# Performance work log

Measured on AMD Instinct MI355X. Metric: run time of the kernel, lower is better.

## Reference

```python
import jax, jax.numpy as jnp
import numpy as np
import math

B, T, D, H, TED = 32, 512, 512, 8, 2048
HD = D // H  # 64


def _ln(x, g, b, eps=1e-5):
    m = jnp.mean(x, axis=-1, keepdims=True)
    v = jnp.mean((x - m) ** 2, axis=-1, keepdims=True)
    return (x - m) * jax.lax.rsqrt(v + eps) * g + b


def setup_inputs() -> dict:
    key = jax.random.key(0)
    ks = jax.random.split(key, 12)
    s = 0.02
    return {
        "x": jax.random.normal(ks[0], (B, T, D), jnp.float32),
        "emb": jax.random.normal(ks[1], (B, TED), jnp.float32),
        "Wq": jax.random.normal(ks[2], (D, D), jnp.float32) * s,
        "Wk": jax.random.normal(ks[3], (D, D), jnp.float32) * s,
        "Wv": jax.random.normal(ks[4], (D, D), jnp.float32) * s,
        "Wsig": jax.random.normal(ks[5], (D, H), jnp.float32) * s,
        "ln1_g": jnp.ones((D,), jnp.float32),
        "ln1_b": jnp.zeros((D,), jnp.float32),
        "emb_W": jax.random.normal(ks[6], (TED, 2 * D), jnp.float32) * s,
        "emb_b": jnp.zeros((2 * D,), jnp.float32),
        "ln2_g": jnp.ones((D,), jnp.float32),
        "ln2_b": jnp.zeros((D,), jnp.float32),
        "out_W": jax.random.normal(ks[7], (D, D), jnp.float32) * s,
        "out_b": jnp.zeros((D,), jnp.float32),
    }


def reference(x, emb, Wq, Wk, Wv, Wsig, ln1_g, ln1_b, emb_W, emb_b,
              ln2_g, ln2_b, out_W, out_b):
    xn = _ln(x, ln1_g, ln1_b)                       # pre-norm, shared by Q/K/V
    q = (xn @ Wq.T).reshape(B, T, H, HD)
    k = (xn @ Wk.T).reshape(B, T, H, HD)
    v = (xn @ Wv.T).reshape(B, T, H, HD)

    # original applies 1/sqrt(D//H) twice (scores and scale) -> effective /HD
    scores = jnp.einsum("bnhd,bmhd->bhnm", q, k) / math.sqrt(HD)
    attention = scores / math.sqrt(D / H)
    series = jax.nn.softmax(attention, axis=-1)     # dropout is identity (p=0/eval)

    sigma = (x @ Wsig).transpose(0, 2, 1)           # B,H,T
    sigma = jax.nn.sigmoid(sigma * 5.0) + 1e-5
    sigma = jnp.power(3.0, sigma) - 1.0             # B,H,T
    sigma4 = sigma[..., None]                       # B,H,T,1 (broadcast over last T)

    idx = jnp.arange(T, dtype=jnp.float32)
    dist = jnp.abs(idx[:, None] - idx[None, :])     # T,T
    prior = jnp.exp(-(dist ** 2) / (2.0 * sigma4 ** 2)) / (
        math.sqrt(2.0 * math.pi) * sigma4)          # B,H,T,T

    y = jnp.einsum("bhnm,bmhd->bnhd", series, v).reshape(B, T, D)

    # StylizationBlock
    emb_out = jax.nn.silu(emb) @ emb_W + emb_b      # B,2D
    scale, shift = jnp.split(emb_out[:, None, :], 2, axis=2)
    h = _ln(y, ln2_g, ln2_b) * (1.0 + scale) + shift
    h = jax.nn.silu(h) @ out_W.T + out_b
    y = x + h

    sigma_full = jnp.broadcast_to(sigma4, (B, H, T, T))
    return (y, series, prior, sigma_full)
```

## Files before the change

### kernel.cpp

```cpp
#include <hip/hip_runtime.h>
#include <cstdint>
#include <cstddef>


typedef __attribute__((ext_vector_type(8))) __bf16 bf16x8;
typedef __attribute__((ext_vector_type(4))) float f32x4;

#define MFMA16(a, b, c) __builtin_amdgcn_mfma_f32_16x16x32_bf16((a), (b), (c), 0, 0, 0)

__device__ __forceinline__ void gload_lds16(const void* g, void* l) {
  __builtin_amdgcn_global_load_lds(
      (const __attribute__((address_space(1))) unsigned int*)g,
      (__attribute__((address_space(3))) unsigned int*)l, 16, 0, 0);
}

__device__ __forceinline__ float wave_sum(float v) {
#pragma unroll
  for (int off = 32; off; off >>= 1) v += __shfl_xor(v, off);
  return v;
}

__global__ void k_convert(const float* __restrict__ Wq, const float* __restrict__ Wk,
                          const float* __restrict__ Wv, const float* __restrict__ Wo,
                          __bf16* __restrict__ wqkv, __bf16* __restrict__ wout,
                          float* __restrict__ embacc) {
  int i = blockIdx.x * 256 + threadIdx.x;
  float v;
  if (i < 262144)      v = Wq[i];
  else if (i < 524288) v = Wk[i - 262144];
  else                 v = Wv[i - 524288];
  wqkv[i] = (__bf16)v;
  if (i < 262144) wout[i] = (__bf16)Wo[i];
  if (i < 32768)  embacc[i] = 0.f;
}

__global__ void k_ln1_sigma(const float* __restrict__ x, const float* __restrict__ g,
                            const float* __restrict__ be, const float* __restrict__ Wsig,
                            __bf16* __restrict__ xn, float* __restrict__ sig) {
  int tid = threadIdx.x, w = tid >> 6, l = tid & 63;
  int row = blockIdx.x * 4 + w;
  const float* xr = x + (size_t)row * 512 + l * 8;
  f32x4 x0 = *(const f32x4*)xr, x1 = *(const f32x4*)(xr + 4);
  float s = 0.f, s2 = 0.f;
#pragma unroll
  for (int i = 0; i < 8; i++) { float v = (i < 4) ? x0[i] : x1[i - 4]; s += v; s2 += v * v; }
  s = wave_sum(s); s2 = wave_sum(s2);
  float m = s * (1.f / 512.f);
  float rstd = rsqrtf(s2 * (1.f / 512.f) - m * m + 1e-5f);
  const float* gr = g + l * 8; const float* br = be + l * 8;
  f32x4 g0 = *(const f32x4*)gr, g1 = *(const f32x4*)(gr + 4);
  f32x4 b0 = *(const f32x4*)br, b1 = *(const f32x4*)(br + 4);
  bf16x8 o;
#pragma unroll
  for (int i = 0; i < 8; i++) {
    float xv = (i < 4) ? x0[i] : x1[i - 4];
    float gv = (i < 4) ? g0[i] : g1[i - 4];
    float bv = (i < 4) ? b0[i] : b1[i - 4];
    o[i] = (__bf16)((xv - m) * rstd * gv + bv);
  }
  *(bf16x8*)(xn + (size_t)row * 512 + l * 8) = o;
  float u[8] = {0, 0, 0, 0, 0, 0, 0, 0};
#pragma unroll
  for (int jj = 0; jj < 8; jj++) {
    float xv = (jj < 4) ? x0[jj] : x1[jj - 4];
    const float* wr = Wsig + (size_t)(l * 8 + jj) * 8;
    f32x4 w0 = *(const f32x4*)wr, w1 = *(const f32x4*)(wr + 4);
    u[0] += xv * w0[0]; u[1] += xv * w0[1]; u[2] += xv * w0[2]; u[3] += xv * w0[3];
    u[4] += xv * w1[0]; u[5] += xv * w1[1]; u[6] += xv * w1[2]; u[7] += xv * w1[3];
  }
#pragma unroll
  for (int hh = 0; hh < 8; hh++) u[hh] = wave_sum(u[hh]);
  if (l < 8) {
    float us = u[0];
#pragma unroll
    for (int hh = 1; hh < 8; hh++) if (l == hh) us = u[hh];
    float sg = 1.f / (1.f + __expf(-5.f * us)) + 1e-5f;
    float sv = expm1f(sg * 1.0986122886681098f);
    sig[(size_t)row * 8 + l] = sv;
  }
}

template <int EPI>
__global__ void k_gemm128(const __bf16* __restrict__ A, const __bf16* __restrict__ Bw,
                          __bf16* __restrict__ Cb, float* __restrict__ Cf,
                          const float* __restrict__ bias, const float* __restrict__ resid,
                          int ldc, int gridN) {
  int bid = blockIdx.x;
  int jn = bid % gridN, im = bid / gridN;
  int i0 = im * 128, j0 = jn * 128;
  int tid = threadIdx.x, w = tid >> 6, l = tid & 63, q = l >> 4, l15 = l & 15;
  int wm = w >> 1, wn = w & 1;
  __shared__ __attribute__((aligned(16))) __bf16 sAB[16384];
  f32x4 acc[4][4] = {};
  for (int k0 = 0; k0 < 512; k0 += 64) {
    __syncthreads();
#pragma unroll
    for (int i = 0; i < 8; i++) {
      int c = w * 8 + i;
      if (c < 16) {
        int rb = c >> 1, ks = c & 1;
        const __bf16* gp = A + (size_t)(i0 + rb * 16 + l15) * 512 + k0 + ks * 32 + q * 8;
        gload_lds16(gp, &sAB[c * 512]);
      } else {
        int cc = c - 16; int cb = cc >> 1, ks = cc & 1;
        const __bf16* gp = Bw + (size_t)(j0 + cb * 16 + l15) * 512 + k0 + ks * 32 + q * 8;
        gload_lds16(gp, &sAB[8192 + cc * 512]);
      }
    }
    __syncthreads();
#pragma unroll
    for (int ks = 0; ks < 2; ks++) {
      bf16x8 af[4], bfr[4];
#pragma unroll
      for (int r4 = 0; r4 < 4; r4++) af[r4] = *(const bf16x8*)&sAB[((wm * 4 + r4) * 2 + ks) * 512 + l * 8];
#pragma unroll
      for (int c4 = 0; c4 < 4; c4++) bfr[c4] = *(const bf16x8*)&sAB[8192 + ((wn * 4 + c4) * 2 + ks) * 512 + l * 8];
#pragma unroll
      for (int r4 = 0; r4 < 4; r4++)
#pragma unroll
        for (int c4 = 0; c4 < 4; c4++)
          acc[r4][c4] = MFMA16(af[r4], bfr[c4], acc[r4][c4]);
    }
  }
#pragma unroll
  for (int r4 = 0; r4 < 4; r4++) {
#pragma unroll
    for (int c4 = 0; c4 < 4; c4++) {
      int j = j0 + wn * 64 + c4 * 16 + l15;
      int ib = i0 + wm * 64 + r4 * 16 + q * 4;
#pragma unroll
      for (int r = 0; r < 4; r++) {
        size_t off = (size_t)(ib + r) * ldc + j;
        if (EPI == 0) Cb[off] = (__bf16)acc[r4][c4][r];
        else          Cf[off] = acc[r4][c4][r] + bias[j] + resid[off];
      }
    }
  }
}

__global__ void k_vtrans(const __bf16* __restrict__ qkv, __bf16* __restrict__ vt) {
  int bid = blockIdx.x;
  int mt = bid & 7, bh = bid >> 3;
  int b = bh >> 3, h = bh & 7;
  __shared__ __bf16 tile[64 * 73];
  int tid = threadIdx.x;
  int row = tid >> 3, c8 = (tid & 7) * 8;
#pragma unroll
  for (int p = 0; p < 2; p++) {
    int rr = row + p * 32;
    int m = mt * 64 + rr;
    bf16x8 v = *(const bf16x8*)(qkv + (size_t)(b * 512 + m) * 1536 + 1024 + h * 64 + c8);
#pragma unroll
    for (int j = 0; j < 8; j++) tile[rr * 73 + c8 + j] = v[j];
  }
  __syncthreads();
  int m8 = (tid & 7) * 8;
#pragma unroll
  for (int p = 0; p < 2; p++) {
    int d = (tid >> 3) + p * 32;
    bf16x8 v;
#pragma unroll
    for (int j = 0; j < 8; j++) v[j] = tile[(m8 + j) * 73 + d];
    *(bf16x8*)(vt + ((size_t)(b * 8 + h) * 64 + d) * 512 + mt * 64 + m8) = v;
  }
}

__global__ __launch_bounds__(256) void k_attn(const __bf16* __restrict__ qkv,
                                              const __bf16* __restrict__ vt,
                                              float* __restrict__ series,
                                              float* __restrict__ yout) {
  int bid = blockIdx.x;
  int bh = bid >> 2, rq = bid & 3;
  int b = bh >> 3, h = bh & 7;
  int tid = threadIdx.x, w = tid >> 6, l = tid & 63, q = l >> 4, l15 = l & 15;
  int n0 = rq * 128 + w * 32;
  __shared__ __attribute__((aligned(16))) __bf16 sK[8192];
  __shared__ __attribute__((aligned(16))) __bf16 sV[8192];
  __shared__ __attribute__((aligned(16))) __bf16 sP[8704];
  const float SC = 0.015625f;
  bf16x8 qf[2][2];
#pragma unroll
  for (int rb = 0; rb < 2; rb++)
#pragma unroll
    for (int ks = 0; ks < 2; ks++)
      qf[rb][ks] = *(const bf16x8*)(qkv + (size_t)(b * 512 + n0 + rb * 16 + l15) * 1536 + h * 64 + ks * 32 + q * 8);

  float rs0[4] = {0, 0, 0, 0}, rs1[4] = {0, 0, 0, 0};
  for (int mt = 0; mt < 4; mt++) {
    __syncthreads();
#pragma unroll
    for (int i = 0; i < 4; i++) {
      int c = w * 4 + i; int mb = c >> 1, ks = c & 1;
      const __bf16* gp = qkv + (size_t)(b * 512 + mt * 128 + mb * 16 + l15) * 1536 + 512 + h * 64 + ks * 32 + q * 8;
      gload_lds16(gp, &sK[c * 512]);
    }
    __syncthreads();
#pragma unroll
    for (int mb = 0; mb < 8; mb++) {
      f32x4 a0 = {0, 0, 0, 0}, a1 = {0, 0, 0, 0};
#pragma unroll
      for (int ks = 0; ks < 2; ks++) {
        bf16x8 kf = *(const bf16x8*)&sK[(mb * 2 + ks) * 512 + l * 8];
        a0 = MFMA16(qf[0][ks], kf, a0);
        a1 = MFMA16(qf[1][ks], kf, a1);
      }
#pragma unroll
      for (int r = 0; r < 4; r++) { rs0[r] += __expf(a0[r] * SC); rs1[r] += __expf(a1[r] * SC); }
    }
  }
  float inv0[4], inv1[4];
#pragma unroll
  for (int r = 0; r < 4; r++) {
    float v0 = rs0[r], v1 = rs1[r];
#pragma unroll
    for (int off = 8; off; off >>= 1) { v0 += __shfl_xor(v0, off); v1 += __shfl_xor(v1, off); }
    inv0[r] = 1.f / v0; inv1[r] = 1.f / v1;
  }
  f32x4 yacc[2][4] = {};
  size_t serb = (size_t)bh * 512 * 512;
  __bf16* pw = &sP[w * 2176];
  for (int mt = 0; mt < 4; mt++) {
    __syncthreads();
#pragma unroll
    for (int i = 0; i < 4; i++) {
      int c = w * 4 + i; int mb = c >> 1, ks = c & 1;
      const __bf16* gp = qkv + (size_t)(b * 512 + mt * 128 + mb * 16 + l15) * 1536 + 512 + h * 64 + ks * 32 + q * 8;
      gload_lds16(gp, &sK[c * 512]);
    }
#pragma unroll
    for (int i = 0; i < 4; i++) {
      int c = w * 4 + i; int nb = c >> 2, ks = c & 3;
      const __bf16* gp = vt + ((size_t)bh * 64 + nb * 16 + l15) * 512 + mt * 128 + ks * 32 + q * 8;
      gload_lds16(gp, &sV[c * 512]);
    }
    __syncthreads();
#pragma unroll
    for (int rb = 0; rb < 2; rb++) {
#pragma unroll
      for (int mb = 0; mb < 8; mb++) {
        f32x4 a = {0, 0, 0, 0};
#pragma unroll
        for (int ks = 0; ks < 2; ks++) {
          bf16x8 kf = *(const bf16x8*)&sK[(mb * 2 + ks) * 512 + l * 8];
          a = MFMA16(qf[rb][ks], kf, a);
        }
        int m = mt * 128 + mb * 16 + l15;
#pragma unroll
        for (int r = 0; r < 4; r++) {
          float p = __expf(a[r] * SC) * (rb ? inv1[r] : inv0[r]);
          int n = n0 + rb * 16 + q * 4 + r;
          series[serb + (size_t)n * 512 + m] = p;
          pw[(q * 4 + r) * 136 + mb * 16 + l15] = (__bf16)p;
        }
      }
      bf16x8 pa[4];
#pragma unroll
      for (int ks = 0; ks < 4; ks++) pa[ks] = *(const bf16x8*)&pw[l15 * 136 + ks * 32 + q * 8];
#pragma unroll
      for (int nb = 0; nb < 4; nb++)
#pragma unroll
        for (int ks = 0; ks < 4; ks++) {
          bf16x8 vf = *(const bf16x8*)&sV[(nb * 4 + ks) * 512 + l * 8];
          yacc[rb][nb] = MFMA16(pa[ks], vf, yacc[rb][nb]);
        }
    }
  }
#pragma unroll
  for (int rb = 0; rb < 2; rb++)
#pragma unroll
    for (int nb = 0; nb < 4; nb++)
#pragma unroll
      for (int r = 0; r < 4; r++) {
        int n = n0 + rb * 16 + q * 4 + r;
        yout[(size_t)(b * 512 + n) * 512 + h * 64 + nb * 16 + l15] = yacc[rb][nb][r];
      }
}

__global__ void k_prior(const float* __restrict__ sig, float* __restrict__ prior,
                        float* __restrict__ sigf) {
  int tid = threadIdx.x;
  int r = blockIdx.x * 2 + (tid >> 7);
  int b = r >> 12, h = (r >> 9) & 7, n = r & 511;
  float sv = sig[(size_t)((b << 9) + n) * 8 + h];
  float c1 = -0.5f / (sv * sv);
  float c2 = 0.3989422804014327f / sv;
  int m0 = (tid & 127) * 4;
  f32x4 pv, s4;
#pragma unroll
  for (int i = 0; i < 4; i++) {
    float d = (float)(n - (m0 + i));
    pv[i] = c2 * __expf(c1 * d * d);
    s4[i] = sv;
  }
  size_t base = (size_t)r * 512 + m0;
  *(f32x4*)(prior + base) = pv;
  *(f32x4*)(sigf + base) = s4;
}

__global__ void k_embmm(const float* __restrict__ emb, const float* __restrict__ embW,
                        float* __restrict__ embacc) {
  int bid = blockIdx.x;
  int jc = bid & 31, tc = bid >> 5;
  int tid = threadIdx.x;
  int jl = tid & 31, bg = tid >> 5;
  __shared__ float se[32][257];
  int t0 = tc * 256;
#pragma unroll
  for (int i = 0; i < 32; i++) {
    int idx = tid + 256 * i;
    int bb = idx >> 8, tt = idx & 255;
    float e = emb[(size_t)bb * 2048 + t0 + tt];
    se[bb][tt] = e / (1.f + __expf(-e));
  }
  __syncthreads();
  int j = jc * 32 + jl;
  float a0 = 0, a1 = 0, a2 = 0, a3 = 0;
  for (int tt = 0; tt < 256; tt += 4) {
    float w0 = embW[(size_t)(t0 + tt) * 1024 + j];
    float w1 = embW[(size_t)(t0 + tt + 1) * 1024 + j];
    float w2 = embW[(size_t)(t0 + tt + 2) * 1024 + j];
    float w3 = embW[(size_t)(t0 + tt + 3) * 1024 + j];
    const float* s0 = &se[bg * 4 + 0][tt];
    const float* s1 = &se[bg * 4 + 1][tt];
    const float* s2 = &se[bg * 4 + 2][tt];
    const float* s3 = &se[bg * 4 + 3][tt];
    a0 += w0 * s0[0] + w1 * s0[1] + w2 * s0[2] + w3 * s0[3];
    a1 += w0 * s1[0] + w1 * s1[1] + w2 * s1[2] + w3 * s1[3];
    a2 += w0 * s2[0] + w1 * s2[1] + w2 * s2[2] + w3 * s2[3];
    a3 += w0 * s3[0] + w1 * s3[1] + w2 * s3[2] + w3 * s3[3];
  }
  atomicAdd(&embacc[(size_t)(bg * 4 + 0) * 1024 + j], a0);
  atomicAdd(&embacc[(size_t)(bg * 4 + 1) * 1024 + j], a1);
  atomicAdd(&embacc[(size_t)(bg * 4 + 2) * 1024 + j], a2);
  atomicAdd(&embacc[(size_t)(bg * 4 + 3) * 1024 + j], a3);
}

__global__ void k_ln2(const float* __restrict__ y, const float* __restrict__ g2,
                      const float* __restrict__ b2, const float* __restrict__ embacc,
                      const float* __restrict__ embb, __bf16* __restrict__ hs) {
  int tid = threadIdx.x, w = tid >> 6, l = tid & 63;
  int row = blockIdx.x * 4 + w;
  int b = row >> 9;
  const float* yr = y + (size_t)row * 512 + l * 8;
  f32x4 y0 = *(const f32x4*)yr, y1 = *(const f32x4*)(yr + 4);
  float s = 0.f, s2 = 0.f;
#pragma unroll
  for (int i = 0; i < 8; i++) { float v = (i < 4) ? y0[i] : y1[i - 4]; s += v; s2 += v * v; }
  s = wave_sum(s); s2 = wave_sum(s2);
  float m = s * (1.f / 512.f);
  float rstd = rsqrtf(s2 * (1.f / 512.f) - m * m + 1e-5f);
  int j = l * 8;
  f32x4 g0 = *(const f32x4*)(g2 + j), g1 = *(const f32x4*)(g2 + j + 4);
  f32x4 bb0 = *(const f32x4*)(b2 + j), bb1 = *(const f32x4*)(b2 + j + 4);
  const float* ea = embacc + (size_t)b * 1024;
  f32x4 sc0 = *(const f32x4*)(ea + j), sc1 = *(const f32x4*)(ea + j + 4);
  f32x4 sh0 = *(const f32x4*)(ea + 512 + j), sh1 = *(const f32x4*)(ea + 512 + j + 4);
  f32x4 e0 = *(const f32x4*)(embb + j), e1 = *(const f32x4*)(embb + j + 4);
  f32x4 f0 = *(const f32x4*)(embb + 512 + j), f1 = *(const f32x4*)(embb + 512 + j + 4);
  bf16x8 o;
#pragma unroll
  for (int i = 0; i < 8; i++) {
    float yv = (i < 4) ? y0[i] : y1[i - 4];
    float gv = (i < 4) ? g0[i] : g1[i - 4];
    float bv = (i < 4) ? bb0[i] : bb1[i - 4];
    float scv = ((i < 4) ? sc0[i] : sc1[i - 4]) + ((i < 4) ? e0[i] : e1[i - 4]);
    float shv = ((i < 4) ? sh0[i] : sh1[i - 4]) + ((i < 4) ? f0[i] : f1[i - 4]);
    float xv = (yv - m) * rstd * gv + bv;
    float v = xv * (1.f + scv) + shv;
    o[i] = (__bf16)(v / (1.f + __expf(-v)));
  }
  *(bf16x8*)(hs + (size_t)row * 512 + l * 8) = o;
}

extern "C" void kernel_launch(void* const* d_in, const int* in_sizes, int n_in,
                              void* d_out, int out_size, void* d_ws, size_t ws_size,
                              hipStream_t stream) {
  const float* x    = (const float*)d_in[0];
  const float* emb  = (const float*)d_in[1];
  const float* Wq   = (const float*)d_in[2];
  const float* Wk   = (const float*)d_in[3];
  const float* Wv   = (const float*)d_in[4];
  const float* Wsig = (const float*)d_in[5];
  const float* ln1g = (const float*)d_in[6];
  const float* ln1b = (const float*)d_in[7];
  const float* embW = (const float*)d_in[8];
  const float* embb = (const float*)d_in[9];
  const float* ln2g = (const float*)d_in[10];
  const float* ln2b = (const float*)d_in[11];
  const float* outW = (const float*)d_in[12];
  const float* outb = (const float*)d_in[13];
  (void)in_sizes; (void)n_in; (void)out_size; (void)ws_size;

  float* out      = (float*)d_out;
  float* o_y      = out;
  float* o_series = out + 8388608;
  float* o_prior  = out + 75497472;
  float* o_sigf   = out + 142606336;

  char* ws = (char*)d_ws;
  __bf16* xn     = (__bf16*)(ws + 0);
  __bf16* wqkv   = (__bf16*)(ws + 16777216);
  __bf16* wout   = (__bf16*)(ws + 18350080);
  float*  sig    = (float*)(ws + 18874368);
  float*  embacc = (float*)(ws + 19398656);
  __bf16* qkv    = (__bf16*)(ws + 19529728);
  __bf16* vt     = (__bf16*)(ws + 69861376);
  float*  yattn  = (float*)(ws + 86638592);
  __bf16* hs     = xn;

  k_convert<<<3072, 256, 0, stream>>>(Wq, Wk, Wv, outW, wqkv, wout, embacc);
  k_ln1_sigma<<<4096, 256, 0, stream>>>(x, ln1g, ln1b, Wsig, xn, sig);
  k_gemm128<0><<<1536, 256, 0, stream>>>(xn, wqkv, qkv, nullptr, nullptr, nullptr, 1536, 12);
  k_vtrans<<<2048, 256, 0, stream>>>(qkv, vt);
  k_attn<<<1024, 256, 0, stream>>>(qkv, vt, o_series, yattn);
  k_prior<<<65536, 256, 0, stream>>>(sig, o_prior, o_sigf);
  k_embmm<<<256, 256, 0, stream>>>(emb, embW, embacc);
  k_ln2<<<4096, 256, 0, stream>>>(yattn, ln2g, ln2b, embacc, embb, hs);
  k_gemm128<1><<<512, 256, 0, stream>>>(hs, wout, nullptr, o_y, outb, x, 512, 4);
}
```

Baseline: 1.058 ms.

## Fuse prior/sigma generation into attention pass and stage GEMM epilogue through LDS

Removes the separate prior kernel and writes the prior and broadcast sigma tensors from inside the attention kernel's compute-bound first pass, so these large stores overlap with MFMA work. Series, prior and sigma stores become nontemporal. The QKV GEMM epilogue now goes through LDS to emit 16-byte coalesced bf16 rows, and the attention output is kept in bf16 to halve the intermediate traffic into LayerNorm 2. This adds register and LDS pressure to the attention kernel and loses a little precision in the attention output.

```diff
diff --git a/kernel.cpp b/kernel.cpp
--- a/kernel.cpp
+++ b/kernel.cpp
@@ -122,17 +122,35 @@
           acc[r4][c4] = MFMA16(af[r4], bfr[c4], acc[r4][c4]);
     }
   }
-#pragma unroll
-  for (int r4 = 0; r4 < 4; r4++) {
-#pragma unroll
-    for (int c4 = 0; c4 < 4; c4++) {
-      int j = j0 + wn * 64 + c4 * 16 + l15;
-      int ib = i0 + wm * 64 + r4 * 16 + q * 4;
-#pragma unroll
-      for (int r = 0; r < 4; r++) {
-        size_t off = (size_t)(ib + r) * ldc + j;
-        if (EPI == 0) Cb[off] = (__bf16)acc[r4][c4][r];
-        else          Cf[off] = acc[r4][c4][r] + bias[j] + resid[off];
+  if (EPI == 0) {
+    __syncthreads();
+    __bf16* ct = &sAB[w * 4096];
+#pragma unroll
+    for (int r4 = 0; r4 < 4; r4++)
+#pragma unroll
+      for (int c4 = 0; c4 < 4; c4++)
+#pragma unroll
+        for (int r = 0; r < 4; r++)
+          ct[(r4 * 16 + q * 4 + r) * 64 + c4 * 16 + l15] = (__bf16)acc[r4][c4][r];
+    int r8 = l >> 3, c8 = (l & 7) * 8;
+#pragma unroll
+    for (int jj = 0; jj < 8; jj++) {
+      int row = r8 + jj * 8;
+      bf16x8 vv = *(const bf16x8*)&ct[row * 64 + c8];
+      *(bf16x8*)&Cb[(size_t)(i0 + wm * 64 + row) * ldc + j0 + wn * 64 + c8] = vv;
+    }
+  } else {
+#pragma unroll
+    for (int r4 = 0; r4 < 4; r4++) {
+#pragma unroll
+      for (int c4 = 0; c4 < 4; c4++) {
+        int j = j0 + wn * 64 + c4 * 16 + l15;
+        int ib = i0 + wm * 64 + r4 * 16 + q * 4;
+#pragma unroll
+        for (int r = 0; r < 4; r++) {
+          size_t off = (size_t)(ib + r) * ldc + j;
+          Cf[off] = acc[r4][c4][r] + bias[j] + resid[off];
+        }
       }
     }
   }
@@ -167,8 +185,11 @@
 
 __global__ __launch_bounds__(256) void k_attn(const __bf16* __restrict__ qkv,
                                               const __bf16* __restrict__ vt,
+                                              const float* __restrict__ sig,
                                               float* __restrict__ series,
-                                              float* __restrict__ yout) {
+                                              float* __restrict__ prior,
+                                              float* __restrict__ sigf,
+                                              __bf16* __restrict__ yout) {
   int bid = blockIdx.x;
   int bh = bid >> 2, rq = bid & 3;
   int b = bh >> 3, h = bh & 7;
@@ -177,7 +198,16 @@
   __shared__ __attribute__((aligned(16))) __bf16 sK[8192];
   __shared__ __attribute__((aligned(16))) __bf16 sV[8192];
   __shared__ __attribute__((aligned(16))) __bf16 sP[8704];
+  __shared__ float sC1[128], sC2[128], sSg[128];
   const float SC = 0.015625f;
+
+  if (tid < 128) {
+    float sv = sig[(size_t)(b * 512 + rq * 128 + tid) * 8 + h];
+    sSg[tid] = sv;
+    sC1[tid] = -0.5f / (sv * sv);
+    sC2[tid] = 0.3989422804014327f / sv;
+  }
+
   bf16x8 qf[2][2];
 #pragma unroll
   for (int rb = 0; rb < 2; rb++)
@@ -186,6 +216,7 @@
       qf[rb][ks] = *(const bf16x8*)(qkv + (size_t)(b * 512 + n0 + rb * 16 + l15) * 1536 + h * 64 + ks * 32 + q * 8);
 
   float rs0[4] = {0, 0, 0, 0}, rs1[4] = {0, 0, 0, 0};
+  int prow = l >> 5, pm4 = (l & 31) * 4;
   for (int mt = 0; mt < 4; mt++) {
     __syncthreads();
 #pragma unroll
@@ -206,6 +237,26 @@
       }
 #pragma unroll
       for (int r = 0; r < 4; r++) { rs0[r] += __expf(a0[r] * SC); rs1[r] += __expf(a1[r] * SC); }
+    }
+    {
+      int mbase = mt * 128 + pm4;
+#pragma unroll
+      for (int j = 0; j < 16; j++) {
+        int rr = 2 * j + prow;
+        int ri = w * 32 + rr;
+        int n = n0 + rr;
+        float c1 = sC1[ri], c2 = sC2[ri], sv = sSg[ri];
+        f32x4 pv, s4;
+#pragma unroll
+        for (int i = 0; i < 4; i++) {
+          float d = (float)(n - (mbase + i));
+          pv[i] = c2 * __expf(c1 * d * d);
+          s4[i] = sv;
+        }
+        size_t off = ((size_t)bh * 512 + n) * 512 + mbase;
+        __builtin_nontemporal_store(pv, (f32x4*)(prior + off));
+        __builtin_nontemporal_store(s4, (f32x4*)(sigf + off));
+      }
     }
   }
   float inv0[4], inv1[4];
@@ -249,7 +300,7 @@
         for (int r = 0; r < 4; r++) {
           float p = __expf(a[r] * SC) * (rb ? inv1[r] : inv0[r]);
           int n = n0 + rb * 16 + q * 4 + r;
-          series[serb + (size_t)n * 512 + m] = p;
+          __builtin_nontemporal_store(p, series + serb + (size_t)n * 512 + m);
           pw[(q * 4 + r) * 136 + mb * 16 + l15] = (__bf16)p;
         }
       }
@@ -272,29 +323,8 @@
 #pragma unroll
       for (int r = 0; r < 4; r++) {
         int n = n0 + rb * 16 + q * 4 + r;
-        yout[(size_t)(b * 512 + n) * 512 + h * 64 + nb * 16 + l15] = yacc[rb][nb][r];
-      }
-}
-
-__global__ void k_prior(const float* __restrict__ sig, float* __restrict__ prior,
-                        float* __restrict__ sigf) {
-  int tid = threadIdx.x;
-  int r = blockIdx.x * 2 + (tid >> 7);
-  int b = r >> 12, h = (r >> 9) & 7, n = r & 511;
-  float sv = sig[(size_t)((b << 9) + n) * 8 + h];
-  float c1 = -0.5f / (sv * sv);
-  float c2 = 0.3989422804014327f / sv;
-  int m0 = (tid & 127) * 4;
-  f32x4 pv, s4;
-#pragma unroll
-  for (int i = 0; i < 4; i++) {
-    float d = (float)(n - (m0 + i));
-    pv[i] = c2 * __expf(c1 * d * d);
-    s4[i] = sv;
-  }
-  size_t base = (size_t)r * 512 + m0;
-  *(f32x4*)(prior + base) = pv;
-  *(f32x4*)(sigf + base) = s4;
+        yout[(size_t)(b * 512 + n) * 512 + h * 64 + nb * 16 + l15] = (__bf16)yacc[rb][nb][r];
+      }
 }
 
 __global__ void k_embmm(const float* __restrict__ emb, const float* __restrict__ embW,
@@ -335,17 +365,17 @@
   atomicAdd(&embacc[(size_t)(bg * 4 + 3) * 1024 + j], a3);
 }
 
-__global__ void k_ln2(const float* __restrict__ y, const float* __restrict__ g2,
+__global__ void k_ln2(const __bf16* __restrict__ y, const float* __restrict__ g2,
                       const float* __restrict__ b2, const float* __restrict__ embacc,
                       const float* __restrict__ embb, __bf16* __restrict__ hs) {
   int tid = threadIdx.x, w = tid >> 6, l = tid & 63;
   int row = blockIdx.x * 4 + w;
   int b = row >> 9;
-  const float* yr = y + (size_t)row * 512 + l * 8;
-  f32x4 y0 = *(const f32x4*)yr, y1 = *(const f32x4*)(yr + 4);
+  bf16x8 yv8 = *(const bf16x8*)(y + (size_t)row * 512 + l * 8);
+  float yv[8];
   float s = 0.f, s2 = 0.f;
 #pragma unroll
-  for (int i = 0; i < 8; i++) { float v = (i < 4) ? y0[i] : y1[i - 4]; s += v; s2 += v * v; }
+  for (int i = 0; i < 8; i++) { yv[i] = (float)yv8[i]; s += yv[i]; s2 += yv[i] * yv[i]; }
   s = wave_sum(s); s2 = wave_sum(s2);
   float m = s * (1.f / 512.f);
   float rstd = rsqrtf(s2 * (1.f / 512.f) - m * m + 1e-5f);
@@ -360,12 +390,11 @@
   bf16x8 o;
 #pragma unroll
   for (int i = 0; i < 8; i++) {
-    float yv = (i < 4) ? y0[i] : y1[i - 4];
     float gv = (i < 4) ? g0[i] : g1[i - 4];
     float bv = (i < 4) ? bb0[i] : bb1[i - 4];
     float scv = ((i < 4) ? sc0[i] : sc1[i - 4]) + ((i < 4) ? e0[i] : e1[i - 4]);
     float shv = ((i < 4) ? sh0[i] : sh1[i - 4]) + ((i < 4) ? f0[i] : f1[i - 4]);
-    float xv = (yv - m) * rstd * gv + bv;
+    float xv = (yv[i] - m) * rstd * gv + bv;
     float v = xv * (1.f + scv) + shv;
     o[i] = (__bf16)(v / (1.f + __expf(-v)));
   }
@@ -405,15 +434,14 @@
   float*  embacc = (float*)(ws + 19398656);
   __bf16* qkv    = (__bf16*)(ws + 19529728);
   __bf16* vt     = (__bf16*)(ws + 69861376);
-  float*  yattn  = (float*)(ws + 86638592);
+  __bf16* yattn  = (__bf16*)(ws + 86638592);
   __bf16* hs     = xn;
 
   k_convert<<<3072, 256, 0, stream>>>(Wq, Wk, Wv, outW, wqkv, wout, embacc);
   k_ln1_sigma<<<4096, 256, 0, stream>>>(x, ln1g, ln1b, Wsig, xn, sig);
   k_gemm128<0><<<1536, 256, 0, stream>>>(xn, wqkv, qkv, nullptr, nullptr, nullptr, 1536, 12);
   k_vtrans<<<2048, 256, 0, stream>>>(qkv, vt);
-  k_attn<<<1024, 256, 0, stream>>>(qkv, vt, o_series, yattn);
-  k_prior<<<65536, 256, 0, stream>>>(sig, o_prior, o_sigf);
+  k_attn<<<1024, 256, 0, stream>>>(qkv, vt, sig, o_series, o_prior, o_sigf, yattn);
   k_embmm<<<256, 256, 0, stream>>>(emb, embW, embacc);
   k_ln2<<<4096, 256, 0, stream>>>(yattn, ln2g, ln2b, embacc, embb, hs);
   k_gemm128<1><<<512, 256, 0, stream>>>(hs, wout, nullptr, o_y, outb, x, 512, 4);
```

After: 1.018 ms. -3.8%, faster.
